# Performance work log

Measured on AMD Instinct MI355X. Metric: run time of the kernel, lower is better.

The kernel has to match this reference:

```python
import jax, jax.numpy as jnp
import numpy as np


def setup_inputs() -> dict:
    key = jax.random.key(0)
    ks = jax.random.split(key, 7)
    S, B, D = 8, 32768, 512
    k = 1.0 / np.sqrt(D)
    u = lambda kk, shape: jax.random.uniform(kk, shape, jnp.float32, -k, k)
    return {
        "x": jax.random.normal(ks[0], (S, B, D), jnp.float32),
        "weight_ih": u(ks[1], (3 * D, D)),
        "weight_hh": u(ks[2], (3 * D, D)),
        "bias_ih": u(ks[3], (3 * D,)),
        "bias_hh": u(ks[4], (3 * D,)),
        "w1": u(ks[5], (D, D)),
        "w2": u(ks[6], (D, D)),
    }


def _gru_cell(xi, h, weight_ih, weight_hh, bias_ih, bias_hh):
    # PyTorch GRUCell gate order: r, z, n
    gi = xi @ weight_ih.T + bias_ih  # [B, 3H]
    gh = h @ weight_hh.T + bias_hh   # [B, 3H]
    i_r, i_z, i_n = jnp.split(gi, 3, axis=-1)
    h_r, h_z, h_n = jnp.split(gh, 3, axis=-1)
    r = jax.nn.sigmoid(i_r + h_r)
    z = jax.nn.sigmoid(i_z + h_z)
    n = jnp.tanh(i_n + r * h_n)
    return (1.0 - z) * n + z * h


def reference(x, weight_ih, weight_hh, bias_ih, bias_hh, w1, w2):
    S, B, _ = x.shape
    H = w1.shape[0]

    def step(carry, inp):
        h, x_prev = carry
        xi, i = inp
        h = _gru_cell(xi, h, weight_ih, weight_hh, bias_ih, bias_hh)
        mixed = h @ w1.T + x_prev @ w2.T  # uses x[i-1]
        h = jnp.where(i % 2 == 1, mixed, h)
        return (h, xi), None

    h0 = jnp.zeros((B, H), x.dtype)  # hn=None -> zeros
    (hn, _), _ = jax.lax.scan(step, (h0, x[0]), (x, jnp.arange(S)))
    return hn
```

## Files before the change

kernel.cpp:

```cpp
#include <hip/hip_runtime.h>


#define BDIM 32768
#define DDIM 512
#define BD (BDIM * DDIM)

typedef short bf16x8 __attribute__((ext_vector_type(8)));
typedef float f32x4 __attribute__((ext_vector_type(4)));
typedef unsigned short u16x8 __attribute__((ext_vector_type(8)));

#define AS1 __attribute__((address_space(1)))
#define AS3 __attribute__((address_space(3)))

__device__ __forceinline__ unsigned short f2bf(float f) {
  union { float f; unsigned u; } v; v.f = f;
  return (unsigned short)((v.u + 0x7fffu + ((v.u >> 16) & 1u)) >> 16);
}
__device__ __forceinline__ float bf2f(unsigned short b) {
  union { unsigned u; float f; } v; v.u = (unsigned)b << 16; return v.f;
}
__device__ __forceinline__ float sigmf(float x) { return 1.0f / (1.0f + __expf(-x)); }
__device__ __forceinline__ float tanhf_(float x) { return 1.0f - 2.0f / (__expf(2.0f * x) + 1.0f); }
__device__ __forceinline__ void bar() { asm volatile("s_barrier" ::: "memory"); }
#define VMCNT(n) asm volatile("s_waitcnt vmcnt(" #n ")" ::: "memory")

template <int N> struct ICt { static constexpr int v = N; };

__global__ void cvt_bf16_all(const float* __restrict__ in, unsigned short* __restrict__ out) {
  const size_t stride = (size_t)gridDim.x * 256;
  for (size_t i = (size_t)blockIdx.x * 256 + threadIdx.x; i < (size_t)BD; i += stride) {
    const size_t o = i * 8;
    const float4 a = *(const float4*)(in + o);
    const float4 b = *(const float4*)(in + o + 4);
    u16x8 v;
    v[0] = f2bf(a.x); v[1] = f2bf(a.y); v[2] = f2bf(a.z); v[3] = f2bf(a.w);
    v[4] = f2bf(b.x); v[5] = f2bf(b.y); v[6] = f2bf(b.z); v[7] = f2bf(b.w);
    *(u16x8*)(out + o) = v;
  }
}

__global__ void prep_w(const float* __restrict__ wih, const float* __restrict__ whh,
                       const float* __restrict__ w1, const float* __restrict__ w2,
                       unsigned short* __restrict__ Wg, unsigned short* __restrict__ Wm) {
  int i = blockIdx.x * 256 + threadIdx.x;
  if (i < 1536 * 1024) {
    const int j = i >> 10, k = i & 1023;
    Wg[i] = f2bf((k < 512) ? wih[j * 512 + k] : whh[j * 512 + (k - 512)]);
  } else {
    i -= 1536 * 1024;
    const int j = i >> 10, k = i & 1023;
    Wm[i] = f2bf((k < 512) ? w1[j * 512 + k] : w2[j * 512 + (k - 512)]);
  }
}

__global__ __launch_bounds__(256, 2) void gru_gates(
    const unsigned short* __restrict__ X, const unsigned short* __restrict__ H,
    const unsigned short* __restrict__ Wg, const float* __restrict__ bih,
    const float* __restrict__ bhh, unsigned short* __restrict__ outB) {
  __shared__ char smem[81920];
  const int t = threadIdx.x;
  const int lane = t & 63, wid = t >> 6;
  const int wm = wid >> 1, wn = wid & 1;
  const int xcd = blockIdx.x & 7, ixc = blockIdx.x >> 3;
  const int bm = xcd * 32 + (ixc >> 3);
  const int bn = ixc & 7;

  f32x4 acc[4][8];
  const f32x4 z4 = {0.f, 0.f, 0.f, 0.f};
#pragma unroll
  for (int a = 0; a < 4; ++a)
#pragma unroll
    for (int b = 0; b < 8; ++b) acc[a][b] = z4;

  const int trow = t >> 3;
  const int tswz = ((t & 7) * 16) ^ ((trow & 7) << 4);
  int asrc[4], bsrc[6];
#pragma unroll
  for (int i = 0; i < 4; ++i) asrc[i] = (bm * 128 + i * 32 + trow) * 1024 + tswz;
#pragma unroll
  for (int j = 0; j < 6; ++j)
    bsrc[j] = ((j >> 1) * 512 + bn * 64 + (j & 1) * 32 + trow) * 2048 + tswz;

  const char* Xc = (const char*)X;
  const char* Hc = (const char*)H;
  const char* Wc = (const char*)Wg;

  auto stage = [&](int tt) {
    const char* Ab = ((tt < 8) ? Xc : Hc) + (tt & 7) * 128;
    const char* Bb = Wc + tt * 128;
    char* dst = smem + (tt & 1) * 40960;
#pragma unroll
    for (int i = 0; i < 4; ++i)
      __builtin_amdgcn_global_load_lds((const AS1 void*)(Ab + asrc[i]),
                                       (AS3 void*)(dst + i * 4096 + t * 16), 16, 0, 0);
#pragma unroll
    for (int j = 0; j < 6; ++j)
      __builtin_amdgcn_global_load_lds((const AS1 void*)(Bb + bsrc[j]),
                                       (AS3 void*)(dst + 16384 + j * 4096 + t * 16), 16, 0, 0);
  };

  const int ar0 = wm * 64 + (lane & 15);
  const int kc0 = (lane >> 4) * 16;

  auto do_tile = [&](int kt, auto nsel) {
    constexpr int NS = decltype(nsel)::v;
    VMCNT(0);
    bar();
    if (kt + 1 < 16) stage(kt + 1);
    const char* pa = smem + (kt & 1) * 40960;
    const char* pb = pa + 16384;
#pragma unroll
    for (int ks = 0; ks < 2; ++ks) {
      bf16x8 av[4], bv[6];
      const int cb = ks * 64 + kc0;
#pragma unroll
      for (int fm = 0; fm < 4; ++fm) {
        const int r = ar0 + fm * 16;
        av[fm] = *(const bf16x8*)(pa + r * 128 + (cb ^ ((r & 7) << 4)));
      }
#pragma unroll
      for (int fn = 0; fn < 6; ++fn) {
        const int r = (fn >> 1) * 64 + wn * 32 + (fn & 1) * 16 + (lane & 15);
        bv[fn] = *(const bf16x8*)(pb + r * 128 + (cb ^ ((r & 7) << 4)));
      }
      __builtin_amdgcn_s_setprio(1);
#pragma unroll
      for (int fn = 0; fn < 6; ++fn) {
        const int ai = (fn < 4) ? fn : NS + (fn - 4);
#pragma unroll
        for (int fm = 0; fm < 4; ++fm)
          acc[fm][ai] = __builtin_amdgcn_mfma_f32_16x16x32_bf16(av[fm], bv[fn],
                                                               acc[fm][ai], 0, 0, 0);
      }
      __builtin_amdgcn_s_setprio(0);
    }
  };

  stage(0);
  for (int kt = 0; kt < 8; ++kt) do_tile(kt, ICt<4>{});
  for (int kt = 8; kt < 16; ++kt) do_tile(kt, ICt<6>{});

  const int erow = (lane >> 4) * 4, ecol = lane & 15;
#pragma unroll
  for (int e = 0; e < 2; ++e) {
    const int d = bn * 64 + wn * 32 + e * 16 + ecol;
    const float br = bih[d] + bhh[d];
    const float bz = bih[512 + d] + bhh[512 + d];
    const float bi = bih[1024 + d];
    const float bh = bhh[1024 + d];
#pragma unroll
    for (int fm = 0; fm < 4; ++fm)
#pragma unroll
      for (int j = 0; j < 4; ++j) {
        const int row = bm * 128 + wm * 64 + fm * 16 + erow + j;
        const size_t off = (size_t)row * 512 + d;
        const float rv = sigmf(acc[fm][0 + e][j] + br);
        const float zv = sigmf(acc[fm][2 + e][j] + bz);
        const float nv = tanhf_(acc[fm][4 + e][j] + bi + rv * (acc[fm][6 + e][j] + bh));
        outB[off] = f2bf((1.0f - zv) * nv + zv * bf2f(H[off]));
      }
  }
}

template <int WF>
__global__ __launch_bounds__(256, 2) void mixed_gemm(
    const unsigned short* __restrict__ Ka, const unsigned short* __restrict__ Kb,
    const unsigned short* __restrict__ Wm,
    unsigned short* __restrict__ outB, float* __restrict__ outF) {
  __shared__ char smem[65536];
  const int t = threadIdx.x;
  const int lane = t & 63, wid = t >> 6;
  const int wm = wid >> 1, wn = wid & 1;
  const int xcd = blockIdx.x & 7, ixc = blockIdx.x >> 3;
  const int bm = xcd * 32 + (ixc >> 2);
  const int bn = ixc & 3;

  f32x4 acc[4][4];
  const f32x4 z4 = {0.f, 0.f, 0.f, 0.f};
#pragma unroll
  for (int a = 0; a < 4; ++a)
#pragma unroll
    for (int b = 0; b < 4; ++b) acc[a][b] = z4;

  const int trow = t >> 3;
  const int tswz = ((t & 7) * 16) ^ ((trow & 7) << 4);
  int asrc[4], bsrc[4];
#pragma unroll
  for (int i = 0; i < 4; ++i) {
    asrc[i] = (bm * 128 + i * 32 + trow) * 1024 + tswz;
    bsrc[i] = (bn * 128 + i * 32 + trow) * 2048 + tswz;
  }
  const char* Kac = (const char*)Ka;
  const char* Kbc = (const char*)Kb;
  const char* Wc = (const char*)Wm;

  auto stage = [&](int tt) {
    const char* Ab = ((tt < 8) ? Kac : Kbc) + (tt & 7) * 128;
    const char* Bb = Wc + tt * 128;
    char* dst = smem + (tt & 1) * 32768;
#pragma unroll
    for (int i = 0; i < 4; ++i)
      __builtin_amdgcn_global_load_lds((const AS1 void*)(Ab + asrc[i]),
                                       (AS3 void*)(dst + i * 4096 + t * 16), 16, 0, 0);
#pragma unroll
    for (int j = 0; j < 4; ++j)
      __builtin_amdgcn_global_load_lds((const AS1 void*)(Bb + bsrc[j]),
                                       (AS3 void*)(dst + 16384 + j * 4096 + t * 16), 16, 0, 0);
  };

  const int ar0 = wm * 64 + (lane & 15);
  const int br0 = wn * 64 + (lane & 15);
  const int kc0 = (lane >> 4) * 16;

  stage(0);
  for (int kt = 0; kt < 16; ++kt) {
    VMCNT(0);
    bar();
    if (kt + 1 < 16) stage(kt + 1);
    const char* pa = smem + (kt & 1) * 32768;
    const char* pb = pa + 16384;
#pragma unroll
    for (int ks = 0; ks < 2; ++ks) {
      bf16x8 av[4], bv[4];
      const int cb = ks * 64 + kc0;
#pragma unroll
      for (int fm = 0; fm < 4; ++fm) {
        const int r = ar0 + fm * 16;
        av[fm] = *(const bf16x8*)(pa + r * 128 + (cb ^ ((r & 7) << 4)));
      }
#pragma unroll
      for (int fn = 0; fn < 4; ++fn) {
        const int r = br0 + fn * 16;
        bv[fn] = *(const bf16x8*)(pb + r * 128 + (cb ^ ((r & 7) << 4)));
      }
      __builtin_amdgcn_s_setprio(1);
#pragma unroll
      for (int fn = 0; fn < 4; ++fn)
#pragma unroll
        for (int fm = 0; fm < 4; ++fm)
          acc[fm][fn] = __builtin_amdgcn_mfma_f32_16x16x32_bf16(av[fm], bv[fn],
                                                               acc[fm][fn], 0, 0, 0);
      __builtin_amdgcn_s_setprio(0);
    }
  }

  const int erow = (lane >> 4) * 4, ecol = lane & 15;
#pragma unroll
  for (int fm = 0; fm < 4; ++fm)
#pragma unroll
    for (int fn = 0; fn < 4; ++fn) {
      const int col = bn * 128 + wn * 64 + fn * 16 + ecol;
#pragma unroll
      for (int j = 0; j < 4; ++j) {
        const int row = bm * 128 + wm * 64 + fm * 16 + erow + j;
        const size_t off = (size_t)row * 512 + col;
        const float v = acc[fm][fn][j];
        if constexpr (WF) outF[off] = v;
        else              outB[off] = f2bf(v);
      }
    }
}

extern "C" void kernel_launch(void* const* d_in, const int* in_sizes, int n_in,
                              void* d_out, int out_size, void* d_ws, size_t ws_size,
                              hipStream_t stream) {
  const float* x   = (const float*)d_in[0];
  const float* wih = (const float*)d_in[1];
  const float* whh = (const float*)d_in[2];
  const float* bih = (const float*)d_in[3];
  const float* bhh = (const float*)d_in[4];
  const float* w1  = (const float*)d_in[5];
  const float* w2  = (const float*)d_in[6];

  char* ws = (char*)d_ws;
  const size_t bd2 = (size_t)BD * 2;
  unsigned short* xall  = (unsigned short*)ws;
  unsigned short* hb[2] = {(unsigned short*)(ws + 8 * bd2),
                           (unsigned short*)(ws + 9 * bd2)};
  unsigned short* Wg = (unsigned short*)(ws + 10 * bd2);
  unsigned short* Wm = Wg + 1536 * 1024;

  hipMemsetAsync(hb[0], 0, bd2, stream);
  cvt_bf16_all<<<2048, 256, 0, stream>>>(x, xall);
  prep_w<<<8192, 256, 0, stream>>>(wih, whh, w1, w2, Wg, Wm);

  int hp = 0;
  for (int i = 0; i < 8; ++i) {
    const unsigned short* xi = xall + (size_t)i * BD;
    gru_gates<<<2048, 256, 0, stream>>>(xi, hb[hp], Wg, bih, bhh, hb[hp ^ 1]);
    hp ^= 1;
    if (i & 1) {
      const unsigned short* xprev = xall + (size_t)(i - 1) * BD;
      if (i == 7)
        mixed_gemm<1><<<1024, 256, 0, stream>>>(hb[hp], xprev, Wm, nullptr, (float*)d_out);
      else
        mixed_gemm<0><<<1024, 256, 0, stream>>>(hb[hp], xprev, Wm, hb[hp ^ 1], nullptr);
      if (i != 7) hp ^= 1;
    }
  }
}
```

Measured before the change: 1.194 ms.

## Fuse fp32-to-bf16 x conversion into GEMM loaders and skip zero-h work in first step

Removes the separate pass that converts all of x to bf16 and the memset of the initial hidden state. The GEMM kernels now read fp32 x directly into registers, pack it to bf16 with v_cvt_pk_bf16_f32 and write it into swizzled LDS, while H and weights still go through direct global-to-LDS loads. The first GRU step gets a specialised variant that skips the K-half for h (h is zero) and the z*h term. This avoids writing and re-reading a bf16 copy of x but doubles the bytes read for x tiles and adds register staging plus an LDS wait inside the main loop.

After: 1.180 ms. About the same (-1.2%).

```diff
diff --git a/kernel.cpp b/kernel.cpp
--- a/kernel.cpp
+++ b/kernel.cpp
@@ -7,7 +7,6 @@
 
 typedef short bf16x8 __attribute__((ext_vector_type(8)));
 typedef float f32x4 __attribute__((ext_vector_type(4)));
-typedef unsigned short u16x8 __attribute__((ext_vector_type(8)));
 
 #define AS1 __attribute__((address_space(1)))
 #define AS3 __attribute__((address_space(3)))
@@ -22,22 +21,16 @@
 __device__ __forceinline__ float sigmf(float x) { return 1.0f / (1.0f + __expf(-x)); }
 __device__ __forceinline__ float tanhf_(float x) { return 1.0f - 2.0f / (__expf(2.0f * x) + 1.0f); }
 __device__ __forceinline__ void bar() { asm volatile("s_barrier" ::: "memory"); }
+#define LGKM0 asm volatile("s_waitcnt lgkmcnt(0)" ::: "memory")
 #define VMCNT(n) asm volatile("s_waitcnt vmcnt(" #n ")" ::: "memory")
 
+__device__ __forceinline__ unsigned cvtpk(float lo, float hi) {
+  unsigned r;
+  asm("v_cvt_pk_bf16_f32 %0, %1, %2" : "=v"(r) : "v"(lo), "v"(hi));
+  return r;
+}
+
 template <int N> struct ICt { static constexpr int v = N; };
-
-__global__ void cvt_bf16_all(const float* __restrict__ in, unsigned short* __restrict__ out) {
-  const size_t stride = (size_t)gridDim.x * 256;
-  for (size_t i = (size_t)blockIdx.x * 256 + threadIdx.x; i < (size_t)BD; i += stride) {
-    const size_t o = i * 8;
-    const float4 a = *(const float4*)(in + o);
-    const float4 b = *(const float4*)(in + o + 4);
-    u16x8 v;
-    v[0] = f2bf(a.x); v[1] = f2bf(a.y); v[2] = f2bf(a.z); v[3] = f2bf(a.w);
-    v[4] = f2bf(b.x); v[5] = f2bf(b.y); v[6] = f2bf(b.z); v[7] = f2bf(b.w);
-    *(u16x8*)(out + o) = v;
-  }
-}
 
 __global__ void prep_w(const float* __restrict__ wih, const float* __restrict__ whh,
                        const float* __restrict__ w1, const float* __restrict__ w2,
@@ -53,11 +46,13 @@
   }
 }
 
+template <int FIRST>
 __global__ __launch_bounds__(256, 2) void gru_gates(
-    const unsigned short* __restrict__ X, const unsigned short* __restrict__ H,
+    const float* __restrict__ Xf, const unsigned short* __restrict__ H,
     const unsigned short* __restrict__ Wg, const float* __restrict__ bih,
     const float* __restrict__ bhh, unsigned short* __restrict__ outB) {
   __shared__ char smem[81920];
+  constexpr int NT = FIRST ? 8 : 16;
   const int t = threadIdx.x;
   const int lane = t & 63, wid = t >> 6;
   const int wm = wid >> 1, wn = wid & 1;
@@ -74,29 +69,58 @@
 
   const int trow = t >> 3;
   const int tswz = ((t & 7) * 16) ^ ((trow & 7) << 4);
-  int asrc[4], bsrc[6];
-#pragma unroll
-  for (int i = 0; i < 4; ++i) asrc[i] = (bm * 128 + i * 32 + trow) * 1024 + tswz;
+  int hsrc[4], bsrc[6], ldsx[4], xsrc[4];
+#pragma unroll
+  for (int i = 0; i < 4; ++i) {
+    hsrc[i] = (bm * 128 + i * 32 + trow) * 1024 + tswz;
+    xsrc[i] = (bm * 128 + i * 32 + trow) * 2048 + (t & 7) * 32;
+    ldsx[i] = (i * 32 + trow) * 128 + tswz;
+  }
 #pragma unroll
   for (int j = 0; j < 6; ++j)
     bsrc[j] = ((j >> 1) * 512 + bn * 64 + (j & 1) * 32 + trow) * 2048 + tswz;
 
-  const char* Xc = (const char*)X;
+  const char* Xc = (const char*)Xf;
   const char* Hc = (const char*)H;
   const char* Wc = (const char*)Wg;
 
-  auto stage = [&](int tt) {
-    const char* Ab = ((tt < 8) ? Xc : Hc) + (tt & 7) * 128;
+  auto stageB = [&](int tt) {
     const char* Bb = Wc + tt * 128;
-    char* dst = smem + (tt & 1) * 40960;
-#pragma unroll
-    for (int i = 0; i < 4; ++i)
-      __builtin_amdgcn_global_load_lds((const AS1 void*)(Ab + asrc[i]),
-                                       (AS3 void*)(dst + i * 4096 + t * 16), 16, 0, 0);
+    char* dst = smem + (tt & 1) * 40960 + 16384;
 #pragma unroll
     for (int j = 0; j < 6; ++j)
       __builtin_amdgcn_global_load_lds((const AS1 void*)(Bb + bsrc[j]),
-                                       (AS3 void*)(dst + 16384 + j * 4096 + t * 16), 16, 0, 0);
+                                       (AS3 void*)(dst + j * 4096 + t * 16), 16, 0, 0);
+  };
+  auto stageAH = [&](int tt) {
+    const char* Ab = Hc + (tt & 7) * 128;
+    char* dst = smem + (tt & 1) * 40960;
+#pragma unroll
+    for (int i = 0; i < 4; ++i)
+      __builtin_amdgcn_global_load_lds((const AS1 void*)(Ab + hsrc[i]),
+                                       (AS3 void*)(dst + i * 4096 + t * 16), 16, 0, 0);
+  };
+
+  float4 xv[4][2];
+  auto loadX = [&](int tt) {
+#pragma unroll
+    for (int i = 0; i < 4; ++i) {
+      const char* p = Xc + xsrc[i] + tt * 256;
+      xv[i][0] = *(const float4*)p;
+      xv[i][1] = *(const float4*)(p + 16);
+    }
+  };
+  auto writeX = [&](int tt) {
+    char* dst = smem + (tt & 1) * 40960;
+#pragma unroll
+    for (int i = 0; i < 4; ++i) {
+      int4 w;
+      w.x = (int)cvtpk(xv[i][0].x, xv[i][0].y);
+      w.y = (int)cvtpk(xv[i][0].z, xv[i][0].w);
+      w.z = (int)cvtpk(xv[i][1].x, xv[i][1].y);
+      w.w = (int)cvtpk(xv[i][1].z, xv[i][1].w);
+      *(int4*)(dst + ldsx[i]) = w;
+    }
   };
 
   const int ar0 = wm * 64 + (lane & 15);
@@ -106,7 +130,12 @@
     constexpr int NS = decltype(nsel)::v;
     VMCNT(0);
     bar();
-    if (kt + 1 < 16) stage(kt + 1);
+    const int nt2 = kt + 1;
+    const bool hasNext = nt2 < NT;
+    const bool nextX = nt2 < 8;
+    if (hasNext && nextX) loadX(nt2);
+    if (hasNext) stageB(nt2);
+    if (hasNext && !nextX) stageAH(nt2);
     const char* pa = smem + (kt & 1) * 40960;
     const char* pb = pa + 16384;
 #pragma unroll
@@ -134,11 +163,17 @@
       }
       __builtin_amdgcn_s_setprio(0);
     }
-  };
-
-  stage(0);
+    if (hasNext && nextX) { writeX(nt2); LGKM0; }
+  };
+
+  loadX(0);
+  writeX(0);
+  LGKM0;
+  stageB(0);
+
   for (int kt = 0; kt < 8; ++kt) do_tile(kt, ICt<4>{});
-  for (int kt = 8; kt < 16; ++kt) do_tile(kt, ICt<6>{});
+  if constexpr (!FIRST)
+    for (int kt = 8; kt < 16; ++kt) do_tile(kt, ICt<6>{});
 
   const int erow = (lane >> 4) * 4, ecol = lane & 15;
 #pragma unroll
@@ -157,14 +192,16 @@
         const float rv = sigmf(acc[fm][0 + e][j] + br);
         const float zv = sigmf(acc[fm][2 + e][j] + bz);
         const float nv = tanhf_(acc[fm][4 + e][j] + bi + rv * (acc[fm][6 + e][j] + bh));
-        outB[off] = f2bf((1.0f - zv) * nv + zv * bf2f(H[off]));
+        float hv = (1.0f - zv) * nv;
+        if constexpr (!FIRST) hv += zv * bf2f(H[off]);
+        outB[off] = f2bf(hv);
       }
   }
 }
 
 template <int WF>
 __global__ __launch_bounds__(256, 2) void mixed_gemm(
-    const unsigned short* __restrict__ Ka, const unsigned short* __restrict__ Kb,
+    const unsigned short* __restrict__ Hb, const float* __restrict__ Xf,
     const unsigned short* __restrict__ Wm,
     unsigned short* __restrict__ outB, float* __restrict__ outF) {
   __shared__ char smem[65536];
@@ -184,39 +221,73 @@
 
   const int trow = t >> 3;
   const int tswz = ((t & 7) * 16) ^ ((trow & 7) << 4);
-  int asrc[4], bsrc[4];
+  int hsrc[4], bsrc[4], ldsx[4], xsrc[4];
 #pragma unroll
   for (int i = 0; i < 4; ++i) {
-    asrc[i] = (bm * 128 + i * 32 + trow) * 1024 + tswz;
+    hsrc[i] = (bm * 128 + i * 32 + trow) * 1024 + tswz;
+    xsrc[i] = (bm * 128 + i * 32 + trow) * 2048 + (t & 7) * 32;
+    ldsx[i] = (i * 32 + trow) * 128 + tswz;
     bsrc[i] = (bn * 128 + i * 32 + trow) * 2048 + tswz;
   }
-  const char* Kac = (const char*)Ka;
-  const char* Kbc = (const char*)Kb;
+  const char* Hc = (const char*)Hb;
+  const char* Xc = (const char*)Xf;
   const char* Wc = (const char*)Wm;
 
-  auto stage = [&](int tt) {
-    const char* Ab = ((tt < 8) ? Kac : Kbc) + (tt & 7) * 128;
+  auto stageB = [&](int tt) {
     const char* Bb = Wc + tt * 128;
-    char* dst = smem + (tt & 1) * 32768;
-#pragma unroll
-    for (int i = 0; i < 4; ++i)
-      __builtin_amdgcn_global_load_lds((const AS1 void*)(Ab + asrc[i]),
-                                       (AS3 void*)(dst + i * 4096 + t * 16), 16, 0, 0);
+    char* dst = smem + (tt & 1) * 32768 + 16384;
 #pragma unroll
     for (int j = 0; j < 4; ++j)
       __builtin_amdgcn_global_load_lds((const AS1 void*)(Bb + bsrc[j]),
-                                       (AS3 void*)(dst + 16384 + j * 4096 + t * 16), 16, 0, 0);
+                                       (AS3 void*)(dst + j * 4096 + t * 16), 16, 0, 0);
+  };
+  auto stageAH = [&](int tt) {
+    const char* Ab = Hc + tt * 128;
+    char* dst = smem + (tt & 1) * 32768;
+#pragma unroll
+    for (int i = 0; i < 4; ++i)
+      __builtin_amdgcn_global_load_lds((const AS1 void*)(Ab + hsrc[i]),
+                                       (AS3 void*)(dst + i * 4096 + t * 16), 16, 0, 0);
+  };
+
+  float4 xv[4][2];
+  auto loadX = [&](int tt) {
+#pragma unroll
+    for (int i = 0; i < 4; ++i) {
+      const char* p = Xc + xsrc[i] + (tt - 8) * 256;
+      xv[i][0] = *(const float4*)p;
+      xv[i][1] = *(const float4*)(p + 16);
+    }
+  };
+  auto writeX = [&](int tt) {
+    char* dst = smem + (tt & 1) * 32768;
+#pragma unroll
+    for (int i = 0; i < 4; ++i) {
+      int4 w;
+      w.x = (int)cvtpk(xv[i][0].x, xv[i][0].y);
+      w.y = (int)cvtpk(xv[i][0].z, xv[i][0].w);
+      w.z = (int)cvtpk(xv[i][1].x, xv[i][1].y);
+      w.w = (int)cvtpk(xv[i][1].z, xv[i][1].w);
+      *(int4*)(dst + ldsx[i]) = w;
+    }
   };
 
   const int ar0 = wm * 64 + (lane & 15);
   const int br0 = wn * 64 + (lane & 15);
   const int kc0 = (lane >> 4) * 16;
 
-  stage(0);
+  stageAH(0);
+  stageB(0);
+
   for (int kt = 0; kt < 16; ++kt) {
     VMCNT(0);
     bar();
-    if (kt + 1 < 16) stage(kt + 1);
+    const int nt2 = kt + 1;
+    const bool hasNext = nt2 < 16;
+    const bool nextX = nt2 >= 8;
+    if (hasNext && nextX) loadX(nt2);
+    if (hasNext) stageB(nt2);
+    if (hasNext && !nextX) stageAH(nt2);
     const char* pa = smem + (kt & 1) * 32768;
     const char* pb = pa + 16384;
 #pragma unroll
@@ -242,6 +313,7 @@
                                                                acc[fm][fn], 0, 0, 0);
       __builtin_amdgcn_s_setprio(0);
     }
+    if (hasNext && nextX) { writeX(nt2); LGKM0; }
   }
 
   const int erow = (lane >> 4) * 4, ecol = lane & 15;
@@ -274,23 +346,20 @@
 
   char* ws = (char*)d_ws;
   const size_t bd2 = (size_t)BD * 2;
-  unsigned short* xall  = (unsigned short*)ws;
-  unsigned short* hb[2] = {(unsigned short*)(ws + 8 * bd2),
-                           (unsigned short*)(ws + 9 * bd2)};
-  unsigned short* Wg = (unsigned short*)(ws + 10 * bd2);
+  unsigned short* hb[2] = {(unsigned short*)ws, (unsigned short*)(ws + bd2)};
+  unsigned short* Wg = (unsigned short*)(ws + 2 * bd2);
   unsigned short* Wm = Wg + 1536 * 1024;
 
-  hipMemsetAsync(hb[0], 0, bd2, stream);
-  cvt_bf16_all<<<2048, 256, 0, stream>>>(x, xall);
   prep_w<<<8192, 256, 0, stream>>>(wih, whh, w1, w2, Wg, Wm);
 
-  int hp = 0;
-  for (int i = 0; i < 8; ++i) {
-    const unsigned short* xi = xall + (size_t)i * BD;
-    gru_gates<<<2048, 256, 0, stream>>>(xi, hb[hp], Wg, bih, bhh, hb[hp ^ 1]);
+  gru_gates<1><<<2048, 256, 0, stream>>>(x, nullptr, Wg, bih, bhh, hb[1]);
+  int hp = 1;
+  for (int i = 1; i < 8; ++i) {
+    const float* xi = x + (size_t)i * BD;
+    gru_gates<0><<<2048, 256, 0, stream>>>(xi, hb[hp], Wg, bih, bhh, hb[hp ^ 1]);
     hp ^= 1;
     if (i & 1) {
-      const unsigned short* xprev = xall + (size_t)(i - 1) * BD;
+      const float* xprev = x + (size_t)(i - 1) * BD;
       if (i == 7)
         mixed_gemm<1><<<1024, 256, 0, stream>>>(hb[hp], xprev, Wm, nullptr, (float*)d_out);
       else
```
